# Performance work log

Measured on AMD Instinct MI355X. Metric: run time of the kernel, lower is better.

## Reference

```python
import jax, jax.numpy as jnp
import numpy as np

NEG = -1000000000.0

def setup_inputs() -> dict:
    key = jax.random.key(0)
    kq, kk, kv = jax.random.split(key, 3)
    B, S, D = 4, 4096, 128
    q = jax.random.normal(kq, (B, S, D), dtype=jnp.float32)
    k = jax.random.normal(kk, (B, S, D), dtype=jnp.float32)
    v = jax.random.normal(kv, (B, S, D), dtype=jnp.float32)
    return {"q": q, "k": k, "v": v, "window_size": 128}

def reference(q, k, v, window_size):
    B, S, D = q.shape
    q = q / jnp.sqrt(jnp.asarray(D, q.dtype))
    # banded mask: keep |i-j| <= window_size-1 (tril(w-1) & triu(-(w-1)))
    idx = jnp.arange(S)
    band = jnp.abs(idx[:, None] - idx[None, :]) <= (window_size - 1)  # [S,S]
    scores = jnp.einsum('bqd,bkd->bqk', q, k)
    scores = jnp.where(band[None, :, :], scores, NEG)
    weights = jax.nn.softmax(scores, axis=-1)
    return jnp.einsum('bqk,bkd->bqd', weights, v)
```

## Files before the change

### kernel.cpp

```cpp
#include <hip/hip_runtime.h>

#define S_LEN  4096
#define D_DIM  128
#define MQ     64
#define KT     64
#define NBATCH 4
#define PS_STR 72

#define KBYTES 16384
#define VBYTES 16384
#define OFF_VB 65536
#define OFF_PB 131072
#define LDS_TOT (131072 + 8 * 16 * PS_STR * 2)

typedef __bf16 bf16x8 __attribute__((ext_vector_type(8)));
typedef float  f32x4  __attribute__((ext_vector_type(4)));
typedef unsigned short u16x4 __attribute__((ext_vector_type(4)));
typedef unsigned short u16x8 __attribute__((ext_vector_type(8)));

__device__ __forceinline__ unsigned short f2bf(float f) {
  return __builtin_bit_cast(unsigned short, static_cast<__bf16>(f));
}
__device__ __forceinline__ float fexp2(float x) { return __builtin_amdgcn_exp2f(x); }
__device__ __forceinline__ bf16x8 ld8(const void* p) {
  return __builtin_bit_cast(bf16x8, *(const u16x8*)p);
}
__device__ __forceinline__ f32x4 mfma16(bf16x8 a, bf16x8 b, f32x4 c) {
  return __builtin_amdgcn_mfma_f32_16x16x32_bf16(a, b, c, 0, 0, 0);
}

__global__ __launch_bounds__(512, 2)
void swa_fwd(const float* __restrict__ Qg, const float* __restrict__ Kg,
             const float* __restrict__ Vg, float* __restrict__ Og)
{
  __shared__ __align__(16) unsigned char lds[LDS_TOT];

  const int tid  = threadIdx.x;
  const int g    = (blockIdx.x & 7) * 32 + (blockIdx.x >> 3);
  const int b    = g >> 6;
  const int q0   = (g & 63) * MQ;
  const size_t base = (size_t)b * S_LEN * D_DIM;

  const int lane = tid & 63;
  const int wv   = tid >> 6;
  const int grp  = wv >> 2;
  const int wvg  = wv & 3;
  const int tg   = tid & 255;
  const int quad = lane >> 4;
  const int l15  = lane & 15;
  const int xorv = (l15 & 7) << 4;

  unsigned char* kbase = lds + grp * 2 * KBYTES;
  unsigned char* vbase = lds + OFF_VB + grp * 2 * VBYTES;
  unsigned short* pw   = (unsigned short*)(lds + OFF_PB) + wv * 16 * PS_STR;

  const int t_lo = (q0 >= 128) ? 0 : (2 - (q0 >> 6));
  const int t_hi = (4032 - q0 >= 128) ? 4 : (2 + ((4032 - q0) >> 6));
  const int ns0 = 3 - t_lo, ns1 = t_hi - 2;
  const int nsteps = ns0 > ns1 ? ns0 : ns1;
  const int ntile  = grp ? ns1 : ns0;
  const int t_beg  = grp ? 3 : t_lo;
  const int kb0    = q0 + (t_beg - 2) * KT;

  const int vd0 = (tg & 31) * 4;
  const int vk0 = (tg >> 5) * 8;
  const int krow0 = tg >> 5;
  const int kcol  = ((tg & 31) * 8) ^ ((krow0 & 7) << 4);

  f32x4 kreg[8], vreg[8];
  if (ntile > 0) {
    const float* gk = Kg + base + (size_t)kb0 * D_DIM;
    const float* gv = Vg + base + (size_t)kb0 * D_DIM;
#pragma unroll
    for (int j = 0; j < 8; ++j) kreg[j] = *(const f32x4*)(gk + j * 1024 + tg * 4);
#pragma unroll
    for (int kk = 0; kk < 8; ++kk)
      vreg[kk] = *(const f32x4*)(gv + (size_t)(vk0 + kk) * D_DIM + vd0);
  }
  bf16x8 aq[4];
  {
    const float qsc = 1.4426950408889634f * 0.08838834764831845f;
    const float* gq = Qg + base + (size_t)(q0 + wvg * 16 + l15) * D_DIM;
#pragma unroll
    for (int ks = 0; ks < 4; ++ks) {
      const f32x4 a0 = *(const f32x4*)(gq + ks * 32 + quad * 8);
      const f32x4 a1 = *(const f32x4*)(gq + ks * 32 + quad * 8 + 4);
      u16x8 y;
#pragma unroll
      for (int e = 0; e < 4; ++e) { y[e] = f2bf(a0[e] * qsc); y[4 + e] = f2bf(a1[e] * qsc); }
      aq[ks] = __builtin_bit_cast(bf16x8, y);
    }
  }

  auto stage = [&](unsigned char* kd, unsigned char* vd) {
#pragma unroll
    for (int j = 0; j < 8; ++j) {
      u16x4 y;
#pragma unroll
      for (int e = 0; e < 4; ++e) y[e] = f2bf(kreg[j][e]);
      *(u16x4*)(kd + (j * 8 + krow0) * 256 + kcol) = y;
    }
#pragma unroll
    for (int e = 0; e < 4; ++e) {
      u16x8 y;
#pragma unroll
      for (int kk = 0; kk < 8; ++kk) y[kk] = f2bf(vreg[kk][e]);
      const int row = vd0 + e;
      *(u16x8*)(vd + row * 128 + ((vk0 * 2) ^ ((row & 7) << 4))) = y;
    }
  };
  if (ntile > 0) stage(kbase, vbase);
  if (ntile > 1) {
    const float* gk = Kg + base + (size_t)(kb0 + KT) * D_DIM;
    const float* gv = Vg + base + (size_t)(kb0 + KT) * D_DIM;
#pragma unroll
    for (int j = 0; j < 8; ++j) kreg[j] = *(const f32x4*)(gk + j * 1024 + tg * 4);
#pragma unroll
    for (int kk = 0; kk < 8; ++kk)
      vreg[kk] = *(const f32x4*)(gv + (size_t)(vk0 + kk) * D_DIM + vd0);
  }
  asm volatile("s_waitcnt lgkmcnt(0)" ::: "memory");
  __builtin_amdgcn_s_barrier();
  __builtin_amdgcn_sched_barrier(0);

  f32x4 acc[9];
#pragma unroll
  for (int d = 0; d < 9; ++d) acc[d] = (f32x4){0.f, 0.f, 0.f, 0.f};
  bf16x8 vones;
  {
    u16x8 y;
#pragma unroll
    for (int e = 0; e < 8; ++e) y[e] = (l15 == 0) ? (unsigned short)0x3F80 : (unsigned short)0;
    vones = __builtin_bit_cast(bf16x8, y);
  }

  for (int step = 0; step < nsteps; ++step) {
    const int  t   = t_beg + step;
    const bool cur = (step < ntile);
    const bool nxt = (step + 1 < ntile);
    const unsigned char* kr = kbase + (step & 1) * KBYTES;
    const unsigned char* vr = vbase + (step & 1) * VBYTES;

    if (cur) {
      int cbLo = 0, cbHi = 3;
      if (t == 0) cbLo = wvg;
      if (t == 4) cbHi = wvg;
      f32x4 sc[4];
      __builtin_amdgcn_s_setprio(1);
#pragma unroll
      for (int cb = 0; cb < 4; ++cb) {
        if (cb < cbLo || cb > cbHi) {
          sc[cb] = (f32x4){-1.0e30f, -1.0e30f, -1.0e30f, -1.0e30f};
          continue;
        }
        f32x4 a = (f32x4){0.f, 0.f, 0.f, 0.f};
#pragma unroll
        for (int ks = 0; ks < 4; ++ks) {
          const bf16x8 kf = ld8(kr + (cb * 16 + l15) * 256 + ((ks * 64 + quad * 16) ^ xorv));
          a = mfma16(aq[ks], kf, a);
        }
        sc[cb] = a;
      }
      __builtin_amdgcn_s_setprio(0);

      if (t == 0 || t == 4) {
        const int off = (t - 2) * KT;
#pragma unroll
        for (int cb = 0; cb < 4; ++cb)
#pragma unroll
          for (int r = 0; r < 4; ++r) {
            const int delta = (wvg * 16 + quad * 4 + r) - (off + cb * 16 + l15);
            if (delta > 127 || delta < -127) sc[cb][r] = -1.0e30f;
          }
      }

#pragma unroll
      for (int cb = 0; cb < 4; ++cb)
#pragma unroll
        for (int r = 0; r < 4; ++r)
          sc[cb][r] = fexp2(sc[cb][r]);

#pragma unroll
      for (int cb = 0; cb < 4; ++cb)
#pragma unroll
        for (int r = 0; r < 4; ++r)
          pw[(quad * 4 + r) * PS_STR + cb * 16 + l15] = f2bf(sc[cb][r]);

      __builtin_amdgcn_s_setprio(1);
#pragma unroll
      for (int ks2 = 0; ks2 < 2; ++ks2) {
        const bf16x8 pf = ld8(&pw[l15 * PS_STR + ks2 * 32 + quad * 8]);
#pragma unroll
        for (int d = 0; d < 8; ++d) {
          const bf16x8 vf = ld8(vr + (d * 16 + l15) * 128 + ((ks2 * 64 + quad * 16) ^ xorv));
          acc[d] = mfma16(pf, vf, acc[d]);
        }
        acc[8] = mfma16(pf, vones, acc[8]);
      }
      __builtin_amdgcn_s_setprio(0);
    }

    if (nxt) {
      stage(kbase + ((step + 1) & 1) * KBYTES, vbase + ((step + 1) & 1) * VBYTES);
      if (step + 2 < ntile) {
        const float* gk = Kg + base + (size_t)(kb0 + (step + 2) * KT) * D_DIM;
        const float* gv = Vg + base + (size_t)(kb0 + (step + 2) * KT) * D_DIM;
#pragma unroll
        for (int j = 0; j < 8; ++j) kreg[j] = *(const f32x4*)(gk + j * 1024 + tg * 4);
#pragma unroll
        for (int kk = 0; kk < 8; ++kk)
          vreg[kk] = *(const f32x4*)(gv + (size_t)(vk0 + kk) * D_DIM + vd0);
      }
    }
    asm volatile("s_waitcnt lgkmcnt(0)" ::: "memory");
    __builtin_amdgcn_s_barrier();
    __builtin_amdgcn_sched_barrier(0);
  }

  float* msc = (float*)lds;
  if (grp == 1) {
    float* p = msc + (wvg * 64 + lane) * 37;
#pragma unroll
    for (int d = 0; d < 9; ++d)
#pragma unroll
      for (int r = 0; r < 4; ++r) p[d * 4 + r] = acc[d][r];
  }
  __syncthreads();
  if (grp == 0) {
    const float* p = msc + (wvg * 64 + lane) * 37;
#pragma unroll
    for (int d = 0; d < 9; ++d)
#pragma unroll
      for (int r = 0; r < 4; ++r) acc[d][r] += p[d * 4 + r];

    float inv[4];
#pragma unroll
    for (int r = 0; r < 4; ++r) {
      const float lr = __shfl(acc[8][r], lane & 48, 64);
      inv[r] = 1.0f / lr;
    }
    float* go = Og + base + (size_t)q0 * D_DIM;
#pragma unroll
    for (int d = 0; d < 8; ++d)
#pragma unroll
      for (int r = 0; r < 4; ++r)
        go[(size_t)(wvg * 16 + quad * 4 + r) * D_DIM + d * 16 + l15] = acc[d][r] * inv[r];
  }
}

extern "C" void kernel_launch(void* const* d_in, const int* in_sizes, int n_in,
                              void* d_out, int out_size, void* d_ws, size_t ws_size,
                              hipStream_t stream) {
  const float* q = (const float*)d_in[0];
  const float* k = (const float*)d_in[1];
  const float* v = (const float*)d_in[2];
  float* o = (float*)d_out;
  dim3 grid(NBATCH * (S_LEN / MQ));
  dim3 block(512);
  swa_fwd<<<grid, block, 0, stream>>>(q, k, v, o);
}
```

Measured before the change: 89.30 us.

## Split KV tiles across four wave groups in a 1024-thread block

The block grows from 512 to 1024 threads, so four wave groups each stage and process one 64-key tile in parallel. This replaces the old scheme, where two groups walked their tiles sequentially with register-prefetched double buffering. A fifth edge tile, when present, is handled in a second pass by group 0. Partial numerators and row sums from groups 1-3 are reduced through swizzled LDS. The aim is to cut serial latency per block, at the cost of a higher thread count that caps registers per thread and extra barriers.

New measurement: 88.54 us. About the same (-0.8%).

```diff
diff --git a/kernel.cpp b/kernel.cpp
--- a/kernel.cpp
+++ b/kernel.cpp
@@ -5,13 +5,10 @@
 #define MQ     64
 #define KT     64
 #define NBATCH 4
-#define PS_STR 72
-
-#define KBYTES 16384
-#define VBYTES 16384
-#define OFF_VB 65536
-#define OFF_PB 131072
-#define LDS_TOT (131072 + 8 * 16 * PS_STR * 2)
+
+#define TILE_B  32768
+#define OFF_P   131072
+#define LDS_TOT 151552
 
 typedef __bf16 bf16x8 __attribute__((ext_vector_type(8)));
 typedef float  f32x4  __attribute__((ext_vector_type(4)));
@@ -29,7 +26,7 @@
   return __builtin_amdgcn_mfma_f32_16x16x32_bf16(a, b, c, 0, 0, 0);
 }
 
-__global__ __launch_bounds__(512, 2)
+__global__ __launch_bounds__(1024, 4)
 void swa_fwd(const float* __restrict__ Qg, const float* __restrict__ Kg,
              const float* __restrict__ Vg, float* __restrict__ Og)
 {
@@ -48,35 +45,48 @@
   const int tg   = tid & 255;
   const int quad = lane >> 4;
   const int l15  = lane & 15;
-  const int xorv = (l15 & 7) << 4;
-
-  unsigned char* kbase = lds + grp * 2 * KBYTES;
-  unsigned char* vbase = lds + OFF_VB + grp * 2 * VBYTES;
-  unsigned short* pw   = (unsigned short*)(lds + OFF_PB) + wv * 16 * PS_STR;
+  const int swz  = (l15 & 7) << 4;
+
+  unsigned char* kbuf = lds + grp * TILE_B;
+  unsigned char* vbuf = kbuf + 16384;
+  unsigned short* pw  = (unsigned short*)(lds + OFF_P + wv * 1280);
 
   const int t_lo = (q0 >= 128) ? 0 : (2 - (q0 >> 6));
   const int t_hi = (4032 - q0 >= 128) ? 4 : (2 + ((4032 - q0) >> 6));
-  const int ns0 = 3 - t_lo, ns1 = t_hi - 2;
-  const int nsteps = ns0 > ns1 ? ns0 : ns1;
-  const int ntile  = grp ? ns1 : ns0;
-  const int t_beg  = grp ? 3 : t_lo;
-  const int kb0    = q0 + (t_beg - 2) * KT;
-
+  const int nt   = t_hi - t_lo + 1;
+  const int myt0 = (grp < nt) ? (t_lo + grp) : -1;
+  const int myt1 = (nt == 5 && grp == 0) ? 4 : -1;
+
+  const int vk0 = (tg >> 5) * 8;
   const int vd0 = (tg & 31) * 4;
-  const int vk0 = (tg >> 5) * 8;
-  const int krow0 = tg >> 5;
-  const int kcol  = ((tg & 31) * 8) ^ ((krow0 & 7) << 4);
-
-  f32x4 kreg[8], vreg[8];
-  if (ntile > 0) {
-    const float* gk = Kg + base + (size_t)kb0 * D_DIM;
-    const float* gv = Vg + base + (size_t)kb0 * D_DIM;
-#pragma unroll
-    for (int j = 0; j < 8; ++j) kreg[j] = *(const f32x4*)(gk + j * 1024 + tg * 4);
+
+  auto stage = [&](int kb) {
+    const float* gk = Kg + base + (size_t)kb * D_DIM;
+#pragma unroll
+    for (int j = 0; j < 8; ++j) {
+      const int f = j * 1024 + tg * 4;
+      const f32x4 x = *(const f32x4*)(gk + f);
+      u16x4 y;
+#pragma unroll
+      for (int e = 0; e < 4; ++e) y[e] = f2bf(x[e]);
+      const int key = f >> 7, dim = f & 127;
+      *(u16x4*)(kbuf + key * 256 + ((dim * 2) ^ ((key & 7) << 4))) = y;
+    }
+    const float* gv = Vg + base + (size_t)kb * D_DIM;
+    f32x4 vx[8];
 #pragma unroll
     for (int kk = 0; kk < 8; ++kk)
-      vreg[kk] = *(const f32x4*)(gv + (size_t)(vk0 + kk) * D_DIM + vd0);
-  }
+      vx[kk] = *(const f32x4*)(gv + (size_t)(vk0 + kk) * D_DIM + vd0);
+#pragma unroll
+    for (int e = 0; e < 4; ++e) {
+      u16x8 y;
+#pragma unroll
+      for (int kk = 0; kk < 8; ++kk) y[kk] = f2bf(vx[kk][e]);
+      const int dim = vd0 + e;
+      *(u16x8*)(vbuf + dim * 128 + ((vk0 * 2) ^ ((dim & 7) << 4))) = y;
+    }
+  };
+
   bf16x8 aq[4];
   {
     const float qsc = 1.4426950408889634f * 0.08838834764831845f;
@@ -92,36 +102,7 @@
     }
   }
 
-  auto stage = [&](unsigned char* kd, unsigned char* vd) {
-#pragma unroll
-    for (int j = 0; j < 8; ++j) {
-      u16x4 y;
-#pragma unroll
-      for (int e = 0; e < 4; ++e) y[e] = f2bf(kreg[j][e]);
-      *(u16x4*)(kd + (j * 8 + krow0) * 256 + kcol) = y;
-    }
-#pragma unroll
-    for (int e = 0; e < 4; ++e) {
-      u16x8 y;
-#pragma unroll
-      for (int kk = 0; kk < 8; ++kk) y[kk] = f2bf(vreg[kk][e]);
-      const int row = vd0 + e;
-      *(u16x8*)(vd + row * 128 + ((vk0 * 2) ^ ((row & 7) << 4))) = y;
-    }
-  };
-  if (ntile > 0) stage(kbase, vbase);
-  if (ntile > 1) {
-    const float* gk = Kg + base + (size_t)(kb0 + KT) * D_DIM;
-    const float* gv = Vg + base + (size_t)(kb0 + KT) * D_DIM;
-#pragma unroll
-    for (int j = 0; j < 8; ++j) kreg[j] = *(const f32x4*)(gk + j * 1024 + tg * 4);
-#pragma unroll
-    for (int kk = 0; kk < 8; ++kk)
-      vreg[kk] = *(const f32x4*)(gv + (size_t)(vk0 + kk) * D_DIM + vd0);
-  }
-  asm volatile("s_waitcnt lgkmcnt(0)" ::: "memory");
-  __builtin_amdgcn_s_barrier();
-  __builtin_amdgcn_sched_barrier(0);
+  if (myt0 >= 0) stage(q0 + (myt0 - 2) * KT);
 
   f32x4 acc[9];
 #pragma unroll
@@ -134,105 +115,92 @@
     vones = __builtin_bit_cast(bf16x8, y);
   }
 
-  for (int step = 0; step < nsteps; ++step) {
-    const int  t   = t_beg + step;
-    const bool cur = (step < ntile);
-    const bool nxt = (step + 1 < ntile);
-    const unsigned char* kr = kbase + (step & 1) * KBYTES;
-    const unsigned char* vr = vbase + (step & 1) * VBYTES;
-
-    if (cur) {
-      int cbLo = 0, cbHi = 3;
-      if (t == 0) cbLo = wvg;
-      if (t == 4) cbHi = wvg;
-      f32x4 sc[4];
+  auto compute = [&](int t) {
+    const int kb = q0 + (t - 2) * KT;
+    int cbLo = 0, cbHi = 3;
+    if (t == 0) cbLo = wvg;
+    if (t == 4) cbHi = wvg;
+    f32x4 sc[4];
+    __builtin_amdgcn_s_setprio(1);
+#pragma unroll
+    for (int cb = 0; cb < 4; ++cb) {
+      if (cb < cbLo || cb > cbHi) {
+        sc[cb] = (f32x4){-1.0e30f, -1.0e30f, -1.0e30f, -1.0e30f};
+        continue;
+      }
+      f32x4 a = (f32x4){0.f, 0.f, 0.f, 0.f};
+#pragma unroll
+      for (int ks = 0; ks < 4; ++ks) {
+        const bf16x8 kf = ld8(kbuf + (cb * 16 + l15) * 256 + ((ks * 64 + quad * 16) ^ swz));
+        a = mfma16(aq[ks], kf, a);
+      }
+      sc[cb] = a;
+    }
+    __builtin_amdgcn_s_setprio(0);
+
+    if (t == 0 || t == 4) {
+      const int off = (t - 2) * KT;
+#pragma unroll
+      for (int cb = 0; cb < 4; ++cb)
+#pragma unroll
+        for (int r = 0; r < 4; ++r) {
+          const int delta = (wvg * 16 + quad * 4 + r) - (off + cb * 16 + l15);
+          if (delta > 127 || delta < -127) sc[cb][r] = -1.0e30f;
+        }
+    }
+
+#pragma unroll
+    for (int cb = 0; cb < 4; ++cb)
+#pragma unroll
+      for (int r = 0; r < 4; ++r)
+        sc[cb][r] = fexp2(sc[cb][r]);
+
+#pragma unroll
+    for (int h = 0; h < 2; ++h) {
+      if ((h == 0 && cbLo >= 2) || (h == 1 && cbHi <= 1)) continue;
+#pragma unroll
+      for (int cb = 2 * h; cb < 2 * h + 2; ++cb)
+#pragma unroll
+        for (int r = 0; r < 4; ++r)
+          pw[(quad * 4 + r) * 40 + (cb & 1) * 16 + l15] = f2bf(sc[cb][r]);
+      const bf16x8 pf = ld8(&pw[l15 * 40 + quad * 8]);
       __builtin_amdgcn_s_setprio(1);
 #pragma unroll
-      for (int cb = 0; cb < 4; ++cb) {
-        if (cb < cbLo || cb > cbHi) {
-          sc[cb] = (f32x4){-1.0e30f, -1.0e30f, -1.0e30f, -1.0e30f};
-          continue;
-        }
-        f32x4 a = (f32x4){0.f, 0.f, 0.f, 0.f};
-#pragma unroll
-        for (int ks = 0; ks < 4; ++ks) {
-          const bf16x8 kf = ld8(kr + (cb * 16 + l15) * 256 + ((ks * 64 + quad * 16) ^ xorv));
-          a = mfma16(aq[ks], kf, a);
-        }
-        sc[cb] = a;
+      for (int d = 0; d < 8; ++d) {
+        const bf16x8 vf = ld8(vbuf + (d * 16 + l15) * 128 + ((h * 64 + quad * 16) ^ swz));
+        acc[d] = mfma16(pf, vf, acc[d]);
       }
+      acc[8] = mfma16(pf, vones, acc[8]);
       __builtin_amdgcn_s_setprio(0);
-
-      if (t == 0 || t == 4) {
-        const int off = (t - 2) * KT;
-#pragma unroll
-        for (int cb = 0; cb < 4; ++cb)
-#pragma unroll
-          for (int r = 0; r < 4; ++r) {
-            const int delta = (wvg * 16 + quad * 4 + r) - (off + cb * 16 + l15);
-            if (delta > 127 || delta < -127) sc[cb][r] = -1.0e30f;
-          }
-      }
-
-#pragma unroll
-      for (int cb = 0; cb < 4; ++cb)
-#pragma unroll
-        for (int r = 0; r < 4; ++r)
-          sc[cb][r] = fexp2(sc[cb][r]);
-
-#pragma unroll
-      for (int cb = 0; cb < 4; ++cb)
-#pragma unroll
-        for (int r = 0; r < 4; ++r)
-          pw[(quad * 4 + r) * PS_STR + cb * 16 + l15] = f2bf(sc[cb][r]);
-
-      __builtin_amdgcn_s_setprio(1);
-#pragma unroll
-      for (int ks2 = 0; ks2 < 2; ++ks2) {
-        const bf16x8 pf = ld8(&pw[l15 * PS_STR + ks2 * 32 + quad * 8]);
-#pragma unroll
-        for (int d = 0; d < 8; ++d) {
-          const bf16x8 vf = ld8(vr + (d * 16 + l15) * 128 + ((ks2 * 64 + quad * 16) ^ xorv));
-          acc[d] = mfma16(pf, vf, acc[d]);
-        }
-        acc[8] = mfma16(pf, vones, acc[8]);
-      }
-      __builtin_amdgcn_s_setprio(0);
-    }
-
-    if (nxt) {
-      stage(kbase + ((step + 1) & 1) * KBYTES, vbase + ((step + 1) & 1) * VBYTES);
-      if (step + 2 < ntile) {
-        const float* gk = Kg + base + (size_t)(kb0 + (step + 2) * KT) * D_DIM;
-        const float* gv = Vg + base + (size_t)(kb0 + (step + 2) * KT) * D_DIM;
-#pragma unroll
-        for (int j = 0; j < 8; ++j) kreg[j] = *(const f32x4*)(gk + j * 1024 + tg * 4);
-#pragma unroll
-        for (int kk = 0; kk < 8; ++kk)
-          vreg[kk] = *(const f32x4*)(gv + (size_t)(vk0 + kk) * D_DIM + vd0);
-      }
-    }
-    asm volatile("s_waitcnt lgkmcnt(0)" ::: "memory");
-    __builtin_amdgcn_s_barrier();
-    __builtin_amdgcn_sched_barrier(0);
-  }
-
-  float* msc = (float*)lds;
-  if (grp == 1) {
-    float* p = msc + (wvg * 64 + lane) * 37;
-#pragma unroll
-    for (int d = 0; d < 9; ++d)
-#pragma unroll
-      for (int r = 0; r < 4; ++r) p[d * 4 + r] = acc[d][r];
-  }
-  __syncthreads();
+    }
+  };
+
+  __syncthreads();
+  if (myt0 >= 0) compute(myt0);
+  __syncthreads();
+
+  if (myt1 >= 0) stage(q0 + (myt1 - 2) * KT);
+  if (grp > 0) {
+    const int idx = wvg * 64 + lane;
+#pragma unroll
+    for (int d = 0; d < 8; ++d)
+      *(f32x4*)(kbuf + idx * 128 + ((d * 16) ^ ((lane & 7) << 4))) = acc[d];
+    *(f32x4*)(lds + OFF_P + wv * 1280 + lane * 16) = acc[8];
+  }
+  __syncthreads();
+  if (myt1 >= 0) compute(myt1);
+  __syncthreads();
+
   if (grp == 0) {
-    const float* p = msc + (wvg * 64 + lane) * 37;
-#pragma unroll
-    for (int d = 0; d < 9; ++d)
-#pragma unroll
-      for (int r = 0; r < 4; ++r) acc[d][r] += p[d * 4 + r];
-
+    const int idx = wvg * 64 + lane;
+#pragma unroll
+    for (int sg = 1; sg < 4; ++sg) {
+      const unsigned char* pb = lds + sg * TILE_B;
+#pragma unroll
+      for (int d = 0; d < 8; ++d)
+        acc[d] += *(const f32x4*)(pb + idx * 128 + ((d * 16) ^ ((lane & 7) << 4)));
+      acc[8] += *(const f32x4*)(lds + OFF_P + (sg * 4 + wvg) * 1280 + lane * 16);
+    }
     float inv[4];
 #pragma unroll
     for (int r = 0; r < 4; ++r) {
@@ -256,6 +224,6 @@
   const float* v = (const float*)d_in[2];
   float* o = (float*)d_out;
   dim3 grid(NBATCH * (S_LEN / MQ));
-  dim3 block(512);
+  dim3 block(1024);
   swa_fwd<<<grid, block, 0, stream>>>(q, k, v, o);
 }
```
